# Performance work log

Hardware: AMD Instinct MI355X
Metric: run time of the kernel (lower is better)

Reference implementation:

```python
import jax, jax.numpy as jnp
import numpy as np

B, C, W = 16, 512, 4096
HEADS, HEAD_DIM, GROUPS = 8, 64, 32
HIDDEN = HEADS * HEAD_DIM
EPS = 1e-5


def setup_inputs() -> dict:
    key = jax.random.key(0)
    ks = jax.random.split(key, 3)
    x = jax.random.normal(ks[0], (B, C, W), dtype=jnp.float32)
    # conv1x1 weights (out_ch, in_ch); init scaled like PyTorch kaiming-uniform-ish
    w_qkv = jax.random.normal(ks[1], (3 * HIDDEN, C), dtype=jnp.float32) / np.sqrt(C)
    w_out = jax.random.normal(ks[2], (C, HIDDEN), dtype=jnp.float32) / np.sqrt(HIDDEN)
    return {
        "x": x,
        "gn_w": jnp.ones((C,), jnp.float32),
        "gn_b": jnp.zeros((C,), jnp.float32),
        "w_qkv": w_qkv,
        "b_qkv": jnp.zeros((3 * HIDDEN,), jnp.float32),
        "w_out": w_out,
        "b_out": jnp.zeros((C,), jnp.float32),
    }


def reference(x, gn_w, gn_b, w_qkv, b_qkv, w_out, b_out):
    b, c, w = x.shape
    # GroupNorm over (channels_per_group, width)
    xg = x.reshape(b, GROUPS, -1)
    mu = xg.mean(axis=-1, keepdims=True)
    var = xg.var(axis=-1, keepdims=True)  # biased, matches torch GroupNorm
    xn = ((xg - mu) * jax.lax.rsqrt(var + EPS)).reshape(b, c, w)
    xn = xn * gn_w[None, :, None] + gn_b[None, :, None]
    # 1x1 conv -> qkv
    qkv = jnp.einsum('bcw,oc->bow', xn, w_qkv) + b_qkv[None, :, None]
    qkv = qkv.reshape(b, 3, HEADS, HEAD_DIM, w)
    q, k, v = qkv[:, 0], qkv[:, 1], qkv[:, 2]  # each (b, h, d, n)
    k = jax.nn.softmax(k, axis=-1)  # softmax over sequence positions
    # linear attention: small (d, e) context per head, then project onto q
    context = jnp.einsum('bhdn,bhen->bhde', k, v)
    out = jnp.einsum('bhde,bhdn->bhen', context, q)  # (b, h, d, n)
    out = out.reshape(b, HIDDEN, w)
    return jnp.einsum('bcw,oc->bow', out, w_out) + b_out[None, :, None]
```

## Files before the change

kernel.cpp:

```cpp
#include <hip/hip_runtime.h>
#include <hip/hip_bf16.h>

#define B 16
#define C 512
#define W 4096
#define HEADS 8
#define HD 64
#define GROUPS 32
#define HIDDEN 512
#define OUT3 1536
#define CPG 16
#define GSIZE (CPG * W)
#define EPS 1e-5f

using bf16 = __hip_bfloat16;
typedef __attribute__((ext_vector_type(8))) short short8;
typedef __attribute__((ext_vector_type(4))) float f32x4;

__device__ __forceinline__ float bf_lo(unsigned u) { return __uint_as_float(u << 16); }
__device__ __forceinline__ float bf_hi(unsigned u) { return __uint_as_float(u & 0xffff0000u); }
__device__ __forceinline__ float bf2f(unsigned short s) { return __uint_as_float(((unsigned)s) << 16); }
__device__ __forceinline__ unsigned short f2bf(float f) {
    unsigned u = __float_as_uint(f);
    unsigned r = 0x7fffu + ((u >> 16) & 1u);
    return (unsigned short)((u + r) >> 16);
}
__device__ __forceinline__ unsigned pack2(float a, float b) {
    return (unsigned)f2bf(a) | ((unsigned)f2bf(b) << 16);
}

__device__ __forceinline__ void async16(const ushort* g, ushort* l) {
    __builtin_amdgcn_global_load_lds((const __attribute__((address_space(1))) void*)g,
                                     (__attribute__((address_space(3))) void*)l, 16, 0, 0);
}

#define SBAR                                  \
    do {                                      \
        asm volatile("" ::: "memory");        \
        __builtin_amdgcn_s_barrier();         \
        asm volatile("" ::: "memory");        \
    } while (0)

__global__ __launch_bounds__(256) void gn_stats_kernel(const float* __restrict__ x,
                                                       float2* __restrict__ stats) {
    __shared__ float s1[256], s2[256];
    int bg = blockIdx.x;
    const float4* p4 = (const float4*)(x + (size_t)bg * GSIZE);
    float sum = 0.f, sq = 0.f;
    for (int i = threadIdx.x; i < GSIZE / 4; i += 256) {
        float4 u = p4[i];
        sum += u.x + u.y + u.z + u.w;
        sq += u.x * u.x + u.y * u.y + u.z * u.z + u.w * u.w;
    }
    s1[threadIdx.x] = sum; s2[threadIdx.x] = sq;
    __syncthreads();
    for (int st = 128; st > 0; st >>= 1) {
        if (threadIdx.x < st) {
            s1[threadIdx.x] += s1[threadIdx.x + st];
            s2[threadIdx.x] += s2[threadIdx.x + st];
        }
        __syncthreads();
    }
    if (threadIdx.x == 0) {
        float mean = s1[0] / (float)GSIZE;
        float var = s2[0] / (float)GSIZE - mean * mean;
        stats[bg] = make_float2(mean, rsqrtf(var + EPS));
    }
}

__global__ __launch_bounds__(256) void convw_kernel(const float* __restrict__ s,
                                                    ushort* __restrict__ d, int n4) {
    int i = blockIdx.x * 256 + threadIdx.x;
    if (i >= n4) return;
    float4 v = ((const float4*)s)[i];
    ushort4 o; o.x = f2bf(v.x); o.y = f2bf(v.y); o.z = f2bf(v.z); o.w = f2bf(v.w);
    ((ushort4*)d)[i] = o;
}

__global__ __launch_bounds__(256) void conv_xnt_kernel(
    const float* __restrict__ x, const float* __restrict__ gnw, const float* __restrict__ gnb,
    const float2* __restrict__ stats, ushort* __restrict__ xnT) {
    __shared__ ushort tile[64][68];
    int b = blockIdx.z, c0 = blockIdx.y * 64, w0 = blockIdx.x * 64;
    int t = threadIdx.x;
    int rc = t >> 4, rw = (t & 15) * 4;
#pragma unroll
    for (int p = 0; p < 4; p++) {
        int cl = p * 16 + rc;
        int c = c0 + cl;
        float2 st = stats[b * GROUPS + (c >> 4)];
        float gw = gnw[c], gb = gnb[c];
        float scale = st.y * gw;
        float shift = gb - st.x * scale;
        float4 v = *(const float4*)(x + ((size_t)b * C + c) * W + w0 + rw);
        tile[cl][rw + 0] = f2bf(v.x * scale + shift);
        tile[cl][rw + 1] = f2bf(v.y * scale + shift);
        tile[cl][rw + 2] = f2bf(v.z * scale + shift);
        tile[cl][rw + 3] = f2bf(v.w * scale + shift);
    }
    __syncthreads();
#pragma unroll
    for (int p = 0; p < 4; p++) {
        int wl = p * 16 + rc;
        int cl = (t & 15) * 4;
        ushort4 o;
        o.x = tile[cl + 0][wl]; o.y = tile[cl + 1][wl];
        o.z = tile[cl + 2][wl]; o.w = tile[cl + 3][wl];
        *(ushort4*)(xnT + ((size_t)b * W + w0 + wl) * C + c0 + cl) = o;
    }
}

template <bool BF16_OUT>
__global__ __launch_bounds__(512, 2) void gemm256_kernel(
    const ushort* __restrict__ A, const ushort* __restrict__ Bw,
    const float* __restrict__ bias, void* __restrict__ Dv,
    long aBatch, long dBatch, long bBatch) {
    __shared__ ushort sm[65536];
    const int b = blockIdx.z;
    const int m0 = blockIdx.x * 256, n0 = blockIdx.y * 256;
    const ushort* Ab = A + (size_t)b * aBatch;
    const ushort* Bwb = Bw + (size_t)b * bBatch;
    const int t = threadIdx.x;
    const int lane = t & 63, wid = t >> 6;
    const int wm = wid >> 2, wn = wid & 3;
    const int quad = lane >> 4, lr = lane & 15;

    auto STAGE = [&](const ushort* P, int row0, int kt, int bb, int isB, int h) {
#pragma unroll
        for (int l = 0; l < 2; l++) {
            int f = t + 512 * l;
            int r = f & 127, kq = f >> 7;
            async16(P + (size_t)(row0 + h * 128 + r) * 512 + kt * 64 + kq * 8,
                    &sm[bb * 32768 + isB * 16384 + h * 1024 + kq * 2048 + r * 8]);
        }
    };

    const int NT = 8;
    STAGE(Bwb, n0, 0, 0, 1, 0); STAGE(Bwb, n0, 0, 0, 1, 1);
    STAGE(Ab, m0, 0, 0, 0, 0); STAGE(Ab, m0, 0, 0, 0, 1);
    STAGE(Bwb, n0, 1, 1, 1, 0); STAGE(Bwb, n0, 1, 1, 1, 1);
    STAGE(Ab, m0, 1, 1, 0, 0);
    asm volatile("s_waitcnt vmcnt(6)" ::: "memory");
    SBAR;

    f32x4 acc[8][4] = {};
    for (int kt = 0; kt < NT; kt++) {
        const int bb = kt & 1;
        const ushort* Al = &sm[bb * 32768];
        const ushort* Bl = &sm[bb * 32768 + 16384];
        short8 af[8], bf[8];
#pragma unroll
        for (int j = 0; j < 4; j++) {
            bf[j * 2 + 0] = *(const short8*)&Bl[((0 + quad) * 256 + wn * 64 + j * 16 + lr) * 8];
            bf[j * 2 + 1] = *(const short8*)&Bl[((4 + quad) * 256 + wn * 64 + j * 16 + lr) * 8];
        }
#pragma unroll
        for (int i = 0; i < 8; i++)
            af[i] = *(const short8*)&Al[((0 + quad) * 256 + wm * 128 + i * 16 + lr) * 8];
        if (kt + 1 < NT) STAGE(Ab, m0, kt + 1, bb ^ 1, 0, 1);
        SBAR;
        __builtin_amdgcn_s_setprio(1);
#pragma unroll
        for (int i = 0; i < 8; i++) {
            acc[i][0] = __builtin_amdgcn_mfma_f32_16x16x32_bf16(af[i], bf[0], acc[i][0], 0, 0, 0);
            acc[i][1] = __builtin_amdgcn_mfma_f32_16x16x32_bf16(af[i], bf[2], acc[i][1], 0, 0, 0);
        }
        __builtin_amdgcn_s_setprio(0);
        asm volatile("s_waitcnt lgkmcnt(0)" ::: "memory");
        SBAR;
        if (kt + 2 < NT) STAGE(Bwb, n0, kt + 2, bb, 1, 0);
        SBAR;
        __builtin_amdgcn_s_setprio(1);
#pragma unroll
        for (int i = 0; i < 8; i++) {
            acc[i][2] = __builtin_amdgcn_mfma_f32_16x16x32_bf16(af[i], bf[4], acc[i][2], 0, 0, 0);
            acc[i][3] = __builtin_amdgcn_mfma_f32_16x16x32_bf16(af[i], bf[6], acc[i][3], 0, 0, 0);
        }
        __builtin_amdgcn_s_setprio(0);
        SBAR;
#pragma unroll
        for (int i = 0; i < 8; i++)
            af[i] = *(const short8*)&Al[((4 + quad) * 256 + wm * 128 + i * 16 + lr) * 8];
        if (kt + 2 < NT) STAGE(Bwb, n0, kt + 2, bb, 1, 1);
        SBAR;
        __builtin_amdgcn_s_setprio(1);
#pragma unroll
        for (int i = 0; i < 8; i++) {
            acc[i][0] = __builtin_amdgcn_mfma_f32_16x16x32_bf16(af[i], bf[1], acc[i][0], 0, 0, 0);
            acc[i][1] = __builtin_amdgcn_mfma_f32_16x16x32_bf16(af[i], bf[3], acc[i][1], 0, 0, 0);
        }
        __builtin_amdgcn_s_setprio(0);
        SBAR;
        if (kt + 2 < NT) STAGE(Ab, m0, kt + 2, bb, 0, 0);
        SBAR;
        __builtin_amdgcn_s_setprio(1);
#pragma unroll
        for (int i = 0; i < 8; i++) {
            acc[i][2] = __builtin_amdgcn_mfma_f32_16x16x32_bf16(af[i], bf[5], acc[i][2], 0, 0, 0);
            acc[i][3] = __builtin_amdgcn_mfma_f32_16x16x32_bf16(af[i], bf[7], acc[i][3], 0, 0, 0);
        }
        __builtin_amdgcn_s_setprio(0);
        if (kt + 2 < NT) {
            asm volatile("s_waitcnt vmcnt(6)" ::: "memory");
        } else {
            asm volatile("s_waitcnt vmcnt(0)" ::: "memory");
        }
        SBAR;
    }

    if constexpr (BF16_OUT) {
        ushort* Db = (ushort*)Dv + (size_t)b * dBatch;
        if (n0 < HIDDEN) {
#pragma unroll
            for (int i = 0; i < 8; i++) {
                int mb = m0 + wm * 128 + i * 16 + quad * 4;
#pragma unroll
                for (int j = 0; j < 4; j++) {
                    int n = n0 + wn * 64 + j * 16 + lr;
                    float bv = bias[n];
                    f32x4 v = acc[i][j];
#pragma unroll
                    for (int r = 0; r < 4; r++)
                        Db[(size_t)(mb + r) * HIDDEN + n] = f2bf(v[r] + bv);
                }
            }
        } else {
#pragma unroll
            for (int i = 0; i < 8; i++) {
                int mb = m0 + wm * 128 + i * 16 + quad * 4;
#pragma unroll
                for (int j = 0; j < 4; j++) {
                    int n = n0 + wn * 64 + j * 16 + lr;
                    float bv = bias[n];
                    f32x4 v = acc[i][j];
                    uint2 st;
                    st.x = pack2(v.x + bv, v.y + bv);
                    st.y = pack2(v.z + bv, v.w + bv);
                    *(uint2*)(Db + (size_t)n * W + mb) = st;
                }
            }
        }
    } else {
        float* Db = (float*)Dv + (size_t)b * dBatch;
#pragma unroll
        for (int i = 0; i < 8; i++) {
            int mb = m0 + wm * 128 + i * 16 + quad * 4;
#pragma unroll
            for (int j = 0; j < 4; j++) {
                int n = n0 + wn * 64 + j * 16 + lr;
                float bv = bias[n];
                f32x4 v = acc[i][j];
                float4 st = make_float4(v.x + bv, v.y + bv, v.z + bv, v.w + bv);
                *(float4*)(Db + (size_t)n * W + mb) = st;
            }
        }
    }
}

#define LOADKV(KR, VR, n0_)                                                                  \
    {                                                                                        \
        _Pragma("unroll") for (int i = 0; i < 4; i++) {                                      \
            KR[i] = *(const uint4*)(kbase + (size_t)(i * 16 + lr) * W + (n0_) + quad * 8);   \
            VR[i] = *(const uint4*)(vbase + (size_t)(i * 16 + lr) * W + (n0_) + quad * 8);   \
        }                                                                                    \
    }
#define STEPKV(KR, VR)                                                                       \
    {                                                                                        \
        short8 af[4], bfv[4];                                                                \
        _Pragma("unroll") for (int i = 0; i < 4; i++) {                                      \
            uint4 u = KR[i];                                                                 \
            float e0 = __expf(bf_lo(u.x)), e1 = __expf(bf_hi(u.x));                          \
            float e2 = __expf(bf_lo(u.y)), e3 = __expf(bf_hi(u.y));                          \
            float e4 = __expf(bf_lo(u.z)), e5 = __expf(bf_hi(u.z));                          \
            float e6 = __expf(bf_lo(u.w)), e7 = __expf(bf_hi(u.w));                          \
            psum[i] += e0 + e1 + e2 + e3 + e4 + e5 + e6 + e7;                                \
            uint4 pk;                                                                        \
            pk.x = pack2(e0, e1); pk.y = pack2(e2, e3);                                      \
            pk.z = pack2(e4, e5); pk.w = pack2(e6, e7);                                      \
            af[i] = *(short8*)&pk;                                                           \
            bfv[i] = *(short8*)&VR[i];                                                       \
        }                                                                                    \
        _Pragma("unroll") for (int i = 0; i < 4; i++)                                        \
            _Pragma("unroll") for (int j = 0; j < 4; j++)                                    \
                acc[i][j] = __builtin_amdgcn_mfma_f32_16x16x32_bf16(af[i], bfv[j],           \
                                                                    acc[i][j], 0, 0, 0);     \
    }

__global__ __launch_bounds__(512) void kv_ctx_kernel(const ushort* __restrict__ qkv,
                                                     float* __restrict__ ctx,
                                                     float* __restrict__ sums) {
    __shared__ float ctxS[64][68];
    __shared__ float ssum[64];
    int bh = blockIdx.x;
    int b = bh >> 3, h = bh & 7;
    const ushort* kbase = qkv + ((size_t)b * OUT3 + HIDDEN + h * HD) * W;
    const ushort* vbase = qkv + ((size_t)b * OUT3 + 2 * HIDDEN + h * HD) * W;
    int t = threadIdx.x, lane = t & 63, wv = t >> 6;
    int quad = lane >> 4, lr = lane & 15;

    for (int i = t; i < 64 * 68; i += 512) ((float*)ctxS)[i] = 0.f;
    if (t < 64) ssum[t] = 0.f;
    __syncthreads();

    const int nbase = wv * 512;
    f32x4 acc[4][4] = {};
    float psum[4] = {0.f, 0.f, 0.f, 0.f};
    uint4 ka[4], va[4], kb[4], vb[4];

    LOADKV(ka, va, nbase);
    for (int s = 0; s < 16; s += 2) {
        if (s + 1 < 16) LOADKV(kb, vb, nbase + (s + 1) * 32);
        STEPKV(ka, va);
        if (s + 2 < 16) LOADKV(ka, va, nbase + (s + 2) * 32);
        STEPKV(kb, vb);
    }

#pragma unroll
    for (int i = 0; i < 4; i++)
#pragma unroll
        for (int j = 0; j < 4; j++) {
            f32x4 v = acc[i][j];
#pragma unroll
            for (int r = 0; r < 4; r++)
                atomicAdd(&ctxS[i * 16 + quad * 4 + r][j * 16 + lr], v[r]);
        }
#pragma unroll
    for (int i = 0; i < 4; i++) {
        float v = psum[i];
        v += __shfl_xor(v, 16);
        v += __shfl_xor(v, 32);
        if (quad == 0) atomicAdd(&ssum[i * 16 + lr], v);
    }
    __syncthreads();
    {
        int d = t >> 3, e0 = (t & 7) * 8;
        float4 a = *(const float4*)&ctxS[d][e0];
        float4 c = *(const float4*)&ctxS[d][e0 + 4];
        float* dst = ctx + (size_t)bh * 4096 + d * 64 + e0;
        *(float4*)dst = a;
        *(float4*)(dst + 4) = c;
    }
    if (t < 64) sums[(size_t)bh * 64 + t] = ssum[t];
}

__global__ __launch_bounds__(256) void weff_kernel(const float* __restrict__ wo,
                                                   const float* __restrict__ ctx,
                                                   const float* __restrict__ sums,
                                                   ushort* __restrict__ weff) {
    __shared__ ushort woS[128 * 64];
    __shared__ float ctxS[64][65];
    int cz = blockIdx.x, h = blockIdx.y, b = blockIdx.z;
    int bh = b * 8 + h;
    int t = threadIdx.x;
    for (int f = t; f < 1024; f += 256) {
        int d = f >> 4, c4 = (f & 15) * 4;
        float4 v = *(const float4*)(ctx + (size_t)bh * 4096 + d * 64 + c4);
        ctxS[d][c4 + 0] = v.x; ctxS[d][c4 + 1] = v.y;
        ctxS[d][c4 + 2] = v.z; ctxS[d][c4 + 3] = v.w;
    }
    for (int f = t; f < 1024; f += 256) {
        int cl = f >> 3, e8 = (f & 7) * 8;
        const float4* p = (const float4*)(wo + (size_t)(cz * 128 + cl) * HIDDEN + h * 64 + e8);
        float4 a = p[0], c = p[1];
        uint4 pk;
        pk.x = pack2(a.x, a.y); pk.y = pack2(a.z, a.w);
        pk.z = pack2(c.x, c.y); pk.w = pack2(c.z, c.w);
        *(uint4*)&woS[cl * 64 + e8] = pk;
    }
    __syncthreads();
    int d = t & 63, wvq = t >> 6;
    float pd = 1.0f / sums[(size_t)bh * 64 + d];
    for (int i = 0; i < 32; i++) {
        int cl = wvq * 32 + i;
        float acc = 0.f;
#pragma unroll
        for (int e = 0; e < 64; e++)
            acc += bf2f(woS[cl * 64 + e]) * ctxS[d][e];
        int c = cz * 128 + cl;
        weff[(size_t)b * (HIDDEN * HIDDEN) + (size_t)c * HIDDEN + h * 64 + d] = f2bf(acc * pd);
    }
}

extern "C" void kernel_launch(void* const* d_in, const int* in_sizes, int n_in,
                              void* d_out, int out_size, void* d_ws, size_t ws_size,
                              hipStream_t stream) {
    const float* x   = (const float*)d_in[0];
    const float* gnw = (const float*)d_in[1];
    const float* gnb = (const float*)d_in[2];
    const float* wq  = (const float*)d_in[3];
    const float* bq  = (const float*)d_in[4];
    const float* wo  = (const float*)d_in[5];
    const float* bo  = (const float*)d_in[6];
    float* out = (float*)d_out;

    char* ws = (char*)d_ws;
    ushort* qkv   = (ushort*)ws;
    ushort* xnT   = (ushort*)(ws + 201326592ull);
    ushort* weff  = xnT;
    float*  sums  = (float*)(ws + 209715200ull);
    ushort* wqb   = (ushort*)(ws + 268435456ull);
    float*  ctx   = (float*)(ws + 268435456ull);
    float2* stats = (float2*)(ws + 270532608ull);

    gn_stats_kernel<<<B * GROUPS, 256, 0, stream>>>(x, stats);
    convw_kernel<<<(OUT3 * C / 4 + 255) / 256, 256, 0, stream>>>(wq, wqb, OUT3 * C / 4);
    conv_xnt_kernel<<<dim3(W / 64, C / 64, B), 256, 0, stream>>>(x, gnw, gnb, stats, xnT);
    gemm256_kernel<true><<<dim3(W / 256, OUT3 / 256, B), 512, 0, stream>>>(
        xnT, wqb, bq, qkv, (long)W * C, (long)OUT3 * W, 0L);
    kv_ctx_kernel<<<B * HEADS, 512, 0, stream>>>(qkv, ctx, sums);
    weff_kernel<<<dim3(4, HEADS, B), 256, 0, stream>>>(wo, ctx, sums, weff);
    gemm256_kernel<false><<<dim3(W / 256, C / 256, B), 512, 0, stream>>>(
        qkv, weff, bo, out, (long)OUT3 * W, (long)C * W, (long)HIDDEN * HIDDEN);
}
```

Baseline: 586.1 us.

## Load GEMM operands straight from global memory and split kv_ctx across two slices

The two GEMMs drop their LDS double-buffered async staging, barriers and priority hints, and instead have each wave load its A and B fragments directly from global memory into registers. Separately, kv_ctx now runs two blocks per (batch, head), each covering half the sequence, and combines the partial context and sums with global atomics after new zero-fill kernels clear them. The GEMM change removes LDS traffic and synchronisation but gives up the data sharing between waves and the load/compute overlap. The kv_ctx split doubles parallelism at the cost of extra launches and atomics.

After: 827.6 us. 41.2% more time.

```diff
diff --git a/kernel.cpp b/kernel.cpp
--- a/kernel.cpp
+++ b/kernel.cpp
@@ -29,18 +29,6 @@
     return (unsigned)f2bf(a) | ((unsigned)f2bf(b) << 16);
 }
 
-__device__ __forceinline__ void async16(const ushort* g, ushort* l) {
-    __builtin_amdgcn_global_load_lds((const __attribute__((address_space(1))) void*)g,
-                                     (__attribute__((address_space(3))) void*)l, 16, 0, 0);
-}
-
-#define SBAR                                  \
-    do {                                      \
-        asm volatile("" ::: "memory");        \
-        __builtin_amdgcn_s_barrier();         \
-        asm volatile("" ::: "memory");        \
-    } while (0)
-
 __global__ __launch_bounds__(256) void gn_stats_kernel(const float* __restrict__ x,
                                                        float2* __restrict__ stats) {
     __shared__ float s1[256], s2[256];
@@ -75,6 +63,11 @@
     float4 v = ((const float4*)s)[i];
     ushort4 o; o.x = f2bf(v.x); o.y = f2bf(v.y); o.z = f2bf(v.z); o.w = f2bf(v.w);
     ((ushort4*)d)[i] = o;
+}
+
+__global__ __launch_bounds__(256) void zero_kernel(float* __restrict__ p, int n4) {
+    int i = blockIdx.x * 256 + threadIdx.x;
+    if (i < n4) ((float4*)p)[i] = make_float4(0.f, 0.f, 0.f, 0.f);
 }
 
 __global__ __launch_bounds__(256) void conv_xnt_kernel(
@@ -111,101 +104,49 @@
 }
 
 template <bool BF16_OUT>
-__global__ __launch_bounds__(512, 2) void gemm256_kernel(
+__global__ __launch_bounds__(512, 2) void gemm_reg_kernel(
     const ushort* __restrict__ A, const ushort* __restrict__ Bw,
     const float* __restrict__ bias, void* __restrict__ Dv,
     long aBatch, long dBatch, long bBatch) {
-    __shared__ ushort sm[65536];
     const int b = blockIdx.z;
     const int m0 = blockIdx.x * 256, n0 = blockIdx.y * 256;
-    const ushort* Ab = A + (size_t)b * aBatch;
-    const ushort* Bwb = Bw + (size_t)b * bBatch;
-    const int t = threadIdx.x;
-    const int lane = t & 63, wid = t >> 6;
+    const int lane = threadIdx.x & 63, wid = threadIdx.x >> 6;
     const int wm = wid >> 2, wn = wid & 3;
     const int quad = lane >> 4, lr = lane & 15;
 
-    auto STAGE = [&](const ushort* P, int row0, int kt, int bb, int isB, int h) {
-#pragma unroll
-        for (int l = 0; l < 2; l++) {
-            int f = t + 512 * l;
-            int r = f & 127, kq = f >> 7;
-            async16(P + (size_t)(row0 + h * 128 + r) * 512 + kt * 64 + kq * 8,
-                    &sm[bb * 32768 + isB * 16384 + h * 1024 + kq * 2048 + r * 8]);
-        }
-    };
-
-    const int NT = 8;
-    STAGE(Bwb, n0, 0, 0, 1, 0); STAGE(Bwb, n0, 0, 0, 1, 1);
-    STAGE(Ab, m0, 0, 0, 0, 0); STAGE(Ab, m0, 0, 0, 0, 1);
-    STAGE(Bwb, n0, 1, 1, 1, 0); STAGE(Bwb, n0, 1, 1, 1, 1);
-    STAGE(Ab, m0, 1, 1, 0, 0);
-    asm volatile("s_waitcnt vmcnt(6)" ::: "memory");
-    SBAR;
+    const ushort* Arow = A + (size_t)b * aBatch + (size_t)(m0 + wm * 128 + lr) * 512 + quad * 8;
+    const ushort* Brow = Bw + (size_t)b * bBatch + (size_t)(n0 + wn * 64 + lr) * 512 + quad * 8;
 
     f32x4 acc[8][4] = {};
-    for (int kt = 0; kt < NT; kt++) {
-        const int bb = kt & 1;
-        const ushort* Al = &sm[bb * 32768];
-        const ushort* Bl = &sm[bb * 32768 + 16384];
+#pragma unroll 2
+    for (int kt = 0; kt < 8; kt++) {
+        const int k0 = kt * 64;
         short8 af[8], bf[8];
 #pragma unroll
         for (int j = 0; j < 4; j++) {
-            bf[j * 2 + 0] = *(const short8*)&Bl[((0 + quad) * 256 + wn * 64 + j * 16 + lr) * 8];
-            bf[j * 2 + 1] = *(const short8*)&Bl[((4 + quad) * 256 + wn * 64 + j * 16 + lr) * 8];
+            bf[j * 2 + 0] = *(const short8*)(Brow + (size_t)(j * 16) * 512 + k0);
+            bf[j * 2 + 1] = *(const short8*)(Brow + (size_t)(j * 16) * 512 + k0 + 32);
         }
 #pragma unroll
         for (int i = 0; i < 8; i++)
-            af[i] = *(const short8*)&Al[((0 + quad) * 256 + wm * 128 + i * 16 + lr) * 8];
-        if (kt + 1 < NT) STAGE(Ab, m0, kt + 1, bb ^ 1, 0, 1);
-        SBAR;
-        __builtin_amdgcn_s_setprio(1);
+            af[i] = *(const short8*)(Arow + (size_t)(i * 16) * 512 + k0);
 #pragma unroll
         for (int i = 0; i < 8; i++) {
             acc[i][0] = __builtin_amdgcn_mfma_f32_16x16x32_bf16(af[i], bf[0], acc[i][0], 0, 0, 0);
             acc[i][1] = __builtin_amdgcn_mfma_f32_16x16x32_bf16(af[i], bf[2], acc[i][1], 0, 0, 0);
-        }
-        __builtin_amdgcn_s_setprio(0);
-        asm volatile("s_waitcnt lgkmcnt(0)" ::: "memory");
-        SBAR;
-        if (kt + 2 < NT) STAGE(Bwb, n0, kt + 2, bb, 1, 0);
-        SBAR;
-        __builtin_amdgcn_s_setprio(1);
-#pragma unroll
-        for (int i = 0; i < 8; i++) {
             acc[i][2] = __builtin_amdgcn_mfma_f32_16x16x32_bf16(af[i], bf[4], acc[i][2], 0, 0, 0);
             acc[i][3] = __builtin_amdgcn_mfma_f32_16x16x32_bf16(af[i], bf[6], acc[i][3], 0, 0, 0);
         }
-        __builtin_amdgcn_s_setprio(0);
-        SBAR;
 #pragma unroll
         for (int i = 0; i < 8; i++)
-            af[i] = *(const short8*)&Al[((4 + quad) * 256 + wm * 128 + i * 16 + lr) * 8];
-        if (kt + 2 < NT) STAGE(Bwb, n0, kt + 2, bb, 1, 1);
-        SBAR;
-        __builtin_amdgcn_s_setprio(1);
+            af[i] = *(const short8*)(Arow + (size_t)(i * 16) * 512 + k0 + 32);
 #pragma unroll
         for (int i = 0; i < 8; i++) {
             acc[i][0] = __builtin_amdgcn_mfma_f32_16x16x32_bf16(af[i], bf[1], acc[i][0], 0, 0, 0);
             acc[i][1] = __builtin_amdgcn_mfma_f32_16x16x32_bf16(af[i], bf[3], acc[i][1], 0, 0, 0);
-        }
-        __builtin_amdgcn_s_setprio(0);
-        SBAR;
-        if (kt + 2 < NT) STAGE(Ab, m0, kt + 2, bb, 0, 0);
-        SBAR;
-        __builtin_amdgcn_s_setprio(1);
-#pragma unroll
-        for (int i = 0; i < 8; i++) {
             acc[i][2] = __builtin_amdgcn_mfma_f32_16x16x32_bf16(af[i], bf[5], acc[i][2], 0, 0, 0);
             acc[i][3] = __builtin_amdgcn_mfma_f32_16x16x32_bf16(af[i], bf[7], acc[i][3], 0, 0, 0);
         }
-        __builtin_amdgcn_s_setprio(0);
-        if (kt + 2 < NT) {
-            asm volatile("s_waitcnt vmcnt(6)" ::: "memory");
-        } else {
-            asm volatile("s_waitcnt vmcnt(0)" ::: "memory");
-        }
-        SBAR;
     }
 
     if constexpr (BF16_OUT) {
@@ -291,7 +232,7 @@
                                                      float* __restrict__ sums) {
     __shared__ float ctxS[64][68];
     __shared__ float ssum[64];
-    int bh = blockIdx.x;
+    int bh = blockIdx.x, slice = blockIdx.y;
     int b = bh >> 3, h = bh & 7;
     const ushort* kbase = qkv + ((size_t)b * OUT3 + HIDDEN + h * HD) * W;
     const ushort* vbase = qkv + ((size_t)b * OUT3 + 2 * HIDDEN + h * HD) * W;
@@ -302,16 +243,16 @@
     if (t < 64) ssum[t] = 0.f;
     __syncthreads();
 
-    const int nbase = wv * 512;
+    const int nbase = slice * 2048 + wv * 256;
     f32x4 acc[4][4] = {};
     float psum[4] = {0.f, 0.f, 0.f, 0.f};
     uint4 ka[4], va[4], kb[4], vb[4];
 
     LOADKV(ka, va, nbase);
-    for (int s = 0; s < 16; s += 2) {
-        if (s + 1 < 16) LOADKV(kb, vb, nbase + (s + 1) * 32);
+    for (int s = 0; s < 8; s += 2) {
+        if (s + 1 < 8) LOADKV(kb, vb, nbase + (s + 1) * 32);
         STEPKV(ka, va);
-        if (s + 2 < 16) LOADKV(ka, va, nbase + (s + 2) * 32);
+        if (s + 2 < 8) LOADKV(ka, va, nbase + (s + 2) * 32);
         STEPKV(kb, vb);
     }
 
@@ -334,13 +275,11 @@
     __syncthreads();
     {
         int d = t >> 3, e0 = (t & 7) * 8;
-        float4 a = *(const float4*)&ctxS[d][e0];
-        float4 c = *(const float4*)&ctxS[d][e0 + 4];
         float* dst = ctx + (size_t)bh * 4096 + d * 64 + e0;
-        *(float4*)dst = a;
-        *(float4*)(dst + 4) = c;
-    }
-    if (t < 64) sums[(size_t)bh * 64 + t] = ssum[t];
+#pragma unroll
+        for (int e = 0; e < 8; e++) atomicAdd(dst + e, ctxS[d][e0 + e]);
+    }
+    if (t < 64) atomicAdd(&sums[(size_t)bh * 64 + t], ssum[t]);
 }
 
 __global__ __launch_bounds__(256) void weff_kernel(const float* __restrict__ wo,
@@ -405,10 +344,12 @@
     gn_stats_kernel<<<B * GROUPS, 256, 0, stream>>>(x, stats);
     convw_kernel<<<(OUT3 * C / 4 + 255) / 256, 256, 0, stream>>>(wq, wqb, OUT3 * C / 4);
     conv_xnt_kernel<<<dim3(W / 64, C / 64, B), 256, 0, stream>>>(x, gnw, gnb, stats, xnT);
-    gemm256_kernel<true><<<dim3(W / 256, OUT3 / 256, B), 512, 0, stream>>>(
+    gemm_reg_kernel<true><<<dim3(W / 256, OUT3 / 256, B), 512, 0, stream>>>(
         xnT, wqb, bq, qkv, (long)W * C, (long)OUT3 * W, 0L);
-    kv_ctx_kernel<<<B * HEADS, 512, 0, stream>>>(qkv, ctx, sums);
+    zero_kernel<<<(524288 / 4 + 255) / 256, 256, 0, stream>>>(ctx, 524288 / 4);
+    zero_kernel<<<(8192 / 4 + 255) / 256, 256, 0, stream>>>(sums, 8192 / 4);
+    kv_ctx_kernel<<<dim3(B * HEADS, 2), 512, 0, stream>>>(qkv, ctx, sums);
     weff_kernel<<<dim3(4, HEADS, B), 256, 0, stream>>>(wo, ctx, sums, weff);
-    gemm256_kernel<false><<<dim3(W / 256, C / 256, B), 512, 0, stream>>>(
+    gemm_reg_kernel<false><<<dim3(W / 256, C / 256, B), 512, 0, stream>>>(
         qkv, weff, bo, out, (long)OUT3 * W, (long)C * W, (long)HIDDEN * HIDDEN);
 }
```
